# Kernel optimization log

Measured on AMD Instinct MI355X. Metric: run time of the kernel, lower is better.

## Reference

```python
import jax, jax.numpy as jnp
import numpy as np

B, T, N, C = 1, 2, 10000, 64
H, Co = 4, 64
E = 160000
NEG_SLOPE = 0.2
LN_EPS = 1e-5


def setup_inputs() -> dict:
    key = jax.random.key(0)
    ks = jax.random.split(key, 8)
    s_in = 1.0 / np.sqrt(C)
    s_att = 1.0 / np.sqrt(Co)
    s_proj = 1.0 / np.sqrt(H * Co)
    return {
        "x": jax.random.normal(ks[0], (B, T, N, C), jnp.float32),
        "edge_index": jax.random.randint(ks[1], (2, E), 0, N, dtype=jnp.int32),
        "W_l": jax.random.normal(ks[2], (C, H * Co), jnp.float32) * s_in,
        "b_l": jnp.zeros((H * Co,), jnp.float32),
        "W_r": jax.random.normal(ks[3], (C, H * Co), jnp.float32) * s_in,
        "b_r": jnp.zeros((H * Co,), jnp.float32),
        "att": jax.random.normal(ks[4], (H, Co), jnp.float32) * s_att,
        "bias": jnp.zeros((H * Co,), jnp.float32),
        "W_proj": jax.random.normal(ks[5], (H * Co, Co), jnp.float32) * s_proj,
        "b_proj": jnp.zeros((Co,), jnp.float32),
        "ln_gamma": jnp.ones((Co,), jnp.float32),
        "ln_beta": jnp.zeros((Co,), jnp.float32),
    }


def reference(x, edge_index, W_l, b_l, W_r, b_r, att, bias, W_proj, b_proj, ln_gamma, ln_beta):
    src, dst = edge_index[0], edge_index[1]
    # node transforms: [B,T,N,H,Co]
    x_l = (x @ W_l + b_l).reshape(B, T, N, H, Co)
    x_r = (x @ W_r + b_r).reshape(B, T, N, H, Co)
    # per-edge gathers: [B,T,E,H,Co]
    x_j = x_l[:, :, src]  # source-side features (messages)
    x_i = x_r[:, :, dst]  # target-side features
    m = jax.nn.leaky_relu(x_i + x_j, NEG_SLOPE)
    alpha = jnp.einsum('bteho,ho->bteh', m, att)  # [B,T,E,H]
    # segment softmax over edges grouped by target node (edge axis leading)
    a = jnp.moveaxis(alpha, 2, 0)  # [E,B,T,H]
    amax = jax.lax.stop_gradient(jax.ops.segment_max(a, dst, num_segments=N))
    a = jnp.exp(a - amax[dst])
    denom = jax.ops.segment_sum(a, dst, num_segments=N)
    attn = a / denom[dst]  # [E,B,T,H]
    # weighted messages scattered to target nodes
    msg = jnp.moveaxis(x_j, 2, 0) * attn[..., None]  # [E,B,T,H,Co]
    agg = jax.ops.segment_sum(msg, dst, num_segments=N)  # [N,B,T,H,Co]
    out = jnp.moveaxis(agg, 0, 2).reshape(B, T, N, H * Co) + bias
    x_mha = jax.nn.relu(out)
    # projection + identity residual (in_channels == out_channels)
    x_sam = x_mha @ W_proj + b_proj + x
    mu = jnp.mean(x_sam, axis=-1, keepdims=True)
    var = jnp.var(x_sam, axis=-1, keepdims=True)
    y = (x_sam - mu) * jax.lax.rsqrt(var + LN_EPS) * ln_gamma + ln_beta
    return jax.nn.relu(y)
```

## Files before the change

### kernel.cpp

```cpp
#include <hip/hip_runtime.h>

#define T_  2
#define N_  10000
#define C_  64
#define H_  4
#define Co_ 64
#define E_  160000
#define HC_ 256
#define PAD_ 48
#define NEG_SLOPE 0.2f
#define LN_EPS 1e-5f
#define SCAT_BLOCKS (E_ / 256)
#define GEMM_BLOCKS (T_ * N_ / 32)

__device__ __forceinline__ float lrelu(float v) {
    return fmaxf(v, NEG_SLOPE * v);
}
__device__ __forceinline__ float bf2f(unsigned short u) {
    return __uint_as_float((unsigned)u << 16);
}
__device__ __forceinline__ unsigned short f2bf(float f) {
    const unsigned u = __float_as_uint(f);
    return (unsigned short)((u + 0x7FFFu + ((u >> 16) & 1u)) >> 16);
}
__device__ __forceinline__ float4 u2f4(ushort4 u) {
    return make_float4(bf2f(u.x), bf2f(u.y), bf2f(u.z), bf2f(u.w));
}
__device__ __forceinline__ float red16(float x) {
    x += __int_as_float(__builtin_amdgcn_mov_dpp(__float_as_int(x), 0xB1,  0xF, 0xF, true));
    x += __int_as_float(__builtin_amdgcn_mov_dpp(__float_as_int(x), 0x4E,  0xF, 0xF, true));
    x += __int_as_float(__builtin_amdgcn_mov_dpp(__float_as_int(x), 0x141, 0xF, 0xF, true));
    x += __int_as_float(__builtin_amdgcn_mov_dpp(__float_as_int(x), 0x140, 0xF, 0xF, true));
    return x;
}
__device__ __forceinline__ float edot(const float4 xi, const float4 av, const float4 c) {
    float p =      lrelu(xi.x + c.x) * av.x;
    p = fmaf(lrelu(xi.y + c.y), av.y, p);
    p = fmaf(lrelu(xi.z + c.z), av.z, p);
    p = fmaf(lrelu(xi.w + c.w), av.w, p);
    return p;
}
__device__ __forceinline__ void group_update(
        const float4 xi, const float4 av,
        const float4 c0, const float4 c1, const float4 c2, const float4 c3,
        int k, int cnt, float& m, float& s, float4& acc) {
    float p0 = red16(edot(xi, av, c0));
    float p1 = red16(edot(xi, av, c1));
    float p2 = red16(edot(xi, av, c2));
    float p3 = red16(edot(xi, av, c3));
    if (k + 1 >= cnt) p1 = -INFINITY;
    if (k + 2 >= cnt) p2 = -INFINITY;
    if (k + 3 >= cnt) p3 = -INFINITY;
    const float gm = fmaxf(fmaxf(p0, p1), fmaxf(p2, p3));
    const float mn = fmaxf(m, gm);
    const float sc = __expf(m - mn);
    const float w0 = __expf(p0 - mn);
    const float w1 = __expf(p1 - mn);
    const float w2 = __expf(p2 - mn);
    const float w3 = __expf(p3 - mn);
    s = fmaf(s, sc, w0 + w1 + w2 + w3);
    acc.x = fmaf(acc.x, sc, fmaf(w0, c0.x, fmaf(w1, c1.x, fmaf(w2, c2.x, w3 * c3.x))));
    acc.y = fmaf(acc.y, sc, fmaf(w0, c0.y, fmaf(w1, c1.y, fmaf(w2, c2.y, w3 * c3.y))));
    acc.z = fmaf(acc.z, sc, fmaf(w0, c0.z, fmaf(w1, c1.z, fmaf(w2, c2.z, w3 * c3.z))));
    acc.w = fmaf(acc.w, sc, fmaf(w0, c0.w, fmaf(w1, c1.w, fmaf(w2, c2.w, w3 * c3.w))));
    m = mn;
}

__global__ __launch_bounds__(256) void scat_gemm(
        const int* __restrict__ src, const int* __restrict__ dst,
        int* __restrict__ cursor, unsigned short* __restrict__ perm,
        const float* __restrict__ x, const float* __restrict__ Wl,
        const float* __restrict__ bl, const float* __restrict__ Wr,
        const float* __restrict__ br, unsigned short* __restrict__ xlb,
        float* __restrict__ xr) {
    __shared__ float4 xs[32 * 16];
    const int tid = threadIdx.x;
    if (blockIdx.x < SCAT_BLOCKS) {
        const int e = blockIdx.x * 256 + tid;
        const int d = dst[e];
        const int pos = atomicAdd(&cursor[d], 1);
        if (pos < PAD_) perm[d * PAD_ + pos] = (unsigned short)src[e];
        return;
    }
    const int r0 = (blockIdx.x - SCAT_BLOCKS) * 32;
    xs[tid]       = ((const float4*)(x + (size_t)r0 * C_))[tid];
    xs[256 + tid] = ((const float4*)(x + (size_t)r0 * C_))[256 + tid];
    __syncthreads();

    const int wv    = tid >> 6;
    const int mat   = wv >> 1;
    const int rbase = (wv & 1) << 4;
    const int col4  = tid & 63;
    const float* W  = mat ? Wr : Wl;
    const float4 b4 = ((const float4*)(mat ? br : bl))[col4];

    float4 acc[16];
    #pragma unroll
    for (int r = 0; r < 16; ++r) acc[r] = b4;

    #pragma unroll 2
    for (int c4 = 0; c4 < 16; ++c4) {
        const float4 w0 = ((const float4*)(W + (size_t)(c4 * 4 + 0) * HC_))[col4];
        const float4 w1 = ((const float4*)(W + (size_t)(c4 * 4 + 1) * HC_))[col4];
        const float4 w2 = ((const float4*)(W + (size_t)(c4 * 4 + 2) * HC_))[col4];
        const float4 w3 = ((const float4*)(W + (size_t)(c4 * 4 + 3) * HC_))[col4];
        #pragma unroll
        for (int r = 0; r < 16; ++r) {
            const float4 xv = xs[(rbase + r) * 16 + c4];
            acc[r].x = fmaf(xv.x, w0.x, acc[r].x);
            acc[r].y = fmaf(xv.x, w0.y, acc[r].y);
            acc[r].z = fmaf(xv.x, w0.z, acc[r].z);
            acc[r].w = fmaf(xv.x, w0.w, acc[r].w);
            acc[r].x = fmaf(xv.y, w1.x, acc[r].x);
            acc[r].y = fmaf(xv.y, w1.y, acc[r].y);
            acc[r].z = fmaf(xv.y, w1.z, acc[r].z);
            acc[r].w = fmaf(xv.y, w1.w, acc[r].w);
            acc[r].x = fmaf(xv.z, w2.x, acc[r].x);
            acc[r].y = fmaf(xv.z, w2.y, acc[r].y);
            acc[r].z = fmaf(xv.z, w2.z, acc[r].z);
            acc[r].w = fmaf(xv.z, w2.w, acc[r].w);
            acc[r].x = fmaf(xv.w, w3.x, acc[r].x);
            acc[r].y = fmaf(xv.w, w3.y, acc[r].y);
            acc[r].z = fmaf(xv.w, w3.z, acc[r].z);
            acc[r].w = fmaf(xv.w, w3.w, acc[r].w);
        }
    }
    if (mat) {
        #pragma unroll
        for (int r = 0; r < 16; ++r)
            ((float4*)(xr + (size_t)(r0 + rbase + r) * HC_))[col4] = acc[r];
    } else {
        #pragma unroll
        for (int r = 0; r < 16; ++r) {
            ushort4 u;
            u.x = f2bf(acc[r].x); u.y = f2bf(acc[r].y);
            u.z = f2bf(acc[r].z); u.w = f2bf(acc[r].w);
            ((ushort4*)(xlb + (size_t)(r0 + rbase + r) * HC_))[col4] = u;
        }
    }
}

__global__ __launch_bounds__(256) void node_agg(
        const unsigned short* __restrict__ xlb, const float* __restrict__ xr,
        const float* __restrict__ att, const unsigned short* __restrict__ perm,
        const int* __restrict__ cursor, unsigned short* __restrict__ aggb) {
    const int n    = blockIdx.x * 4 + (threadIdx.x >> 6);
    const int lane = threadIdx.x & 63;
    const int deg  = min(cursor[n], PAD_);
    const float4 av  = ((const float4*)att)[lane];
    const float4 xi0 = ((const float4*)&xr[(size_t)n * HC_])[lane];
    const float4 xi1 = ((const float4*)&xr[((size_t)N_ + n) * HC_])[lane];
    const int myidx  = (lane < deg) ? (int)perm[n * PAD_ + lane] : 0;
    const unsigned short* xl1 = xlb + (size_t)N_ * HC_;

    float m0 = -INFINITY, s0 = 0.f;
    float m1 = -INFINITY, s1 = 0.f;
    float4 a0 = make_float4(0.f, 0.f, 0.f, 0.f);
    float4 a1 = make_float4(0.f, 0.f, 0.f, 0.f);

    ushort4 b00, b01, b02, b03, b10, b11, b12, b13;
    {
        const int i0 = __builtin_amdgcn_readlane(myidx, 0);
        const int i1 = __builtin_amdgcn_readlane(myidx, 1);
        const int i2 = __builtin_amdgcn_readlane(myidx, 2);
        const int i3 = __builtin_amdgcn_readlane(myidx, 3);
        b00 = ((const ushort4*)&xlb[(size_t)i0 * HC_])[lane];
        b01 = ((const ushort4*)&xlb[(size_t)i1 * HC_])[lane];
        b02 = ((const ushort4*)&xlb[(size_t)i2 * HC_])[lane];
        b03 = ((const ushort4*)&xlb[(size_t)i3 * HC_])[lane];
        b10 = ((const ushort4*)&xl1[(size_t)i0 * HC_])[lane];
        b11 = ((const ushort4*)&xl1[(size_t)i1 * HC_])[lane];
        b12 = ((const ushort4*)&xl1[(size_t)i2 * HC_])[lane];
        b13 = ((const ushort4*)&xl1[(size_t)i3 * HC_])[lane];
    }
    for (int k = 0; k < deg; k += 4) {
        const float4 c00 = u2f4(b00), c01 = u2f4(b01), c02 = u2f4(b02), c03 = u2f4(b03);
        const float4 c10 = u2f4(b10), c11 = u2f4(b11), c12 = u2f4(b12), c13 = u2f4(b13);
        if (k + 4 < deg) {
            const int i0 = __builtin_amdgcn_readlane(myidx, k + 4);
            const int i1 = __builtin_amdgcn_readlane(myidx, k + 5);
            const int i2 = __builtin_amdgcn_readlane(myidx, k + 6);
            const int i3 = __builtin_amdgcn_readlane(myidx, k + 7);
            b00 = ((const ushort4*)&xlb[(size_t)i0 * HC_])[lane];
            b01 = ((const ushort4*)&xlb[(size_t)i1 * HC_])[lane];
            b02 = ((const ushort4*)&xlb[(size_t)i2 * HC_])[lane];
            b03 = ((const ushort4*)&xlb[(size_t)i3 * HC_])[lane];
            b10 = ((const ushort4*)&xl1[(size_t)i0 * HC_])[lane];
            b11 = ((const ushort4*)&xl1[(size_t)i1 * HC_])[lane];
            b12 = ((const ushort4*)&xl1[(size_t)i2 * HC_])[lane];
            b13 = ((const ushort4*)&xl1[(size_t)i3 * HC_])[lane];
        }
        group_update(xi0, av, c00, c01, c02, c03, k, deg, m0, s0, a0);
        group_update(xi1, av, c10, c11, c12, c13, k, deg, m1, s1, a1);
    }
    if (deg > 0) {
        float inv = 1.f / s0;
        a0.x *= inv; a0.y *= inv; a0.z *= inv; a0.w *= inv;
        inv = 1.f / s1;
        a1.x *= inv; a1.y *= inv; a1.z *= inv; a1.w *= inv;
    }
    ushort4 o;
    o.x = f2bf(a0.x); o.y = f2bf(a0.y); o.z = f2bf(a0.z); o.w = f2bf(a0.w);
    ((ushort4*)&aggb[(size_t)n * HC_])[lane] = o;
    o.x = f2bf(a1.x); o.y = f2bf(a1.y); o.z = f2bf(a1.z); o.w = f2bf(a1.w);
    ((ushort4*)&aggb[((size_t)N_ + n) * HC_])[lane] = o;
}

__global__ __launch_bounds__(256) void epilogue(
        const unsigned short* __restrict__ aggb, const float* __restrict__ bias,
        const float* __restrict__ Wp, const float* __restrict__ bp,
        const float* __restrict__ x, const float* __restrict__ gamma,
        const float* __restrict__ beta, float* __restrict__ out) {
    __shared__ float sh[32 * HC_];
    const int r0  = blockIdx.x * 32;
    const int tid = threadIdx.x;
    #pragma unroll
    for (int i = 0; i < 8; ++i) {
        const int slot = i * 256 + tid;
        const int r = slot >> 6, f4 = slot & 63;
        const ushort4 u = ((const ushort4*)&aggb[(size_t)(r0 + r) * HC_])[f4];
        const float4 b = ((const float4*)bias)[f4];
        float4 v;
        v.x = fmaxf(bf2f(u.x) + b.x, 0.f); v.y = fmaxf(bf2f(u.y) + b.y, 0.f);
        v.z = fmaxf(bf2f(u.z) + b.z, 0.f); v.w = fmaxf(bf2f(u.w) + b.w, 0.f);
        ((float4*)sh)[slot] = v;
    }
    __syncthreads();
    const int wave = tid >> 6, o = tid & 63;
    const int rbase = wave * 8;
    const float bpo = bp[o];
    float acc[8];
    #pragma unroll
    for (int r = 0; r < 8; ++r)
        acc[r] = bpo + x[(size_t)(r0 + rbase + r) * C_ + o];
    for (int k = 0; k < HC_; k += 4) {
        const float w0 = Wp[(k + 0) * Co_ + o];
        const float w1 = Wp[(k + 1) * Co_ + o];
        const float w2 = Wp[(k + 2) * Co_ + o];
        const float w3 = Wp[(k + 3) * Co_ + o];
        #pragma unroll
        for (int r = 0; r < 8; ++r) {
            const float4 s4 = ((const float4*)&sh[(rbase + r) * HC_])[k >> 2];
            acc[r] = fmaf(s4.x, w0, acc[r]);
            acc[r] = fmaf(s4.y, w1, acc[r]);
            acc[r] = fmaf(s4.z, w2, acc[r]);
            acc[r] = fmaf(s4.w, w3, acc[r]);
        }
    }
    const float go = gamma[o], bo = beta[o];
    #pragma unroll
    for (int r = 0; r < 8; ++r) {
        float s1 = acc[r];
        #pragma unroll
        for (int off = 1; off < 64; off <<= 1) s1 += __shfl_xor(s1, off, 64);
        const float mu = s1 * (1.f / 64.f);
        const float dv = acc[r] - mu;
        float s2 = dv * dv;
        #pragma unroll
        for (int off = 1; off < 64; off <<= 1) s2 += __shfl_xor(s2, off, 64);
        const float var = s2 * (1.f / 64.f);
        const float y = dv * rsqrtf(var + LN_EPS) * go + bo;
        out[(size_t)(r0 + rbase + r) * C_ + o] = fmaxf(y, 0.f);
    }
}

extern "C" void kernel_launch(void* const* d_in, const int* in_sizes, int n_in,
                              void* d_out, int out_size, void* d_ws, size_t ws_size,
                              hipStream_t stream) {
    const float* x    = (const float*)d_in[0];
    const int*   ei   = (const int*)  d_in[1];
    const float* Wl   = (const float*)d_in[2];
    const float* bl   = (const float*)d_in[3];
    const float* Wr   = (const float*)d_in[4];
    const float* br   = (const float*)d_in[5];
    const float* att  = (const float*)d_in[6];
    const float* bias = (const float*)d_in[7];
    const float* Wp   = (const float*)d_in[8];
    const float* bp   = (const float*)d_in[9];
    const float* gam  = (const float*)d_in[10];
    const float* bet  = (const float*)d_in[11];
    const int* src = ei;
    const int* dst = ei + E_;

    char* ws = (char*)d_ws;
    unsigned short* xlb  = (unsigned short*)ws;
    float*          xr   = (float*)(xlb + (size_t)T_ * N_ * HC_);
    unsigned short* aggb = (unsigned short*)(xr + (size_t)T_ * N_ * HC_);
    int*            cursor = (int*)(aggb + (size_t)T_ * N_ * HC_);
    unsigned short* perm   = (unsigned short*)(cursor + N_);

    hipMemsetAsync(cursor, 0, N_ * sizeof(int), stream);
    scat_gemm<<<SCAT_BLOCKS + GEMM_BLOCKS, 256, 0, stream>>>(
        src, dst, cursor, perm, x, Wl, bl, Wr, br, xlb, xr);
    node_agg<<<N_ / 4, 256, 0, stream>>>(xlb, xr, att, perm, cursor, aggb);
    epilogue<<<T_ * N_ / 32, 256, 0, stream>>>(aggb, bias, Wp, bp, x,
                                               gam, bet, (float*)d_out);
}
```

Before: 172.2 us.

## Fuse node aggregation with projection and LayerNorm epilogue into one kernel

Merges node_agg and epilogue into a single node_proj kernel. Each wave now processes two nodes with a combined prefetch pipeline over both nodes' edge groups, then writes the biased, ReLU'd aggregates to shared memory and performs the projection, residual and LayerNorm directly. This removes the bf16 aggb round trip through global memory and one kernel launch. In exchange each wave reads all of Wp for only four rows instead of eight, so weight traffic per output rises. Register pressure also increases, constrained by launch_bounds(256,4).

```diff
diff --git a/kernel.cpp b/kernel.cpp
--- a/kernel.cpp
+++ b/kernel.cpp
@@ -140,127 +140,159 @@
     }
 }
 
-__global__ __launch_bounds__(256) void node_agg(
+__global__ __launch_bounds__(256, 4) void node_proj(
         const unsigned short* __restrict__ xlb, const float* __restrict__ xr,
         const float* __restrict__ att, const unsigned short* __restrict__ perm,
-        const int* __restrict__ cursor, unsigned short* __restrict__ aggb) {
-    const int n    = blockIdx.x * 4 + (threadIdx.x >> 6);
-    const int lane = threadIdx.x & 63;
-    const int deg  = min(cursor[n], PAD_);
-    const float4 av  = ((const float4*)att)[lane];
-    const float4 xi0 = ((const float4*)&xr[(size_t)n * HC_])[lane];
-    const float4 xi1 = ((const float4*)&xr[((size_t)N_ + n) * HC_])[lane];
-    const int myidx  = (lane < deg) ? (int)perm[n * PAD_ + lane] : 0;
-    const unsigned short* xl1 = xlb + (size_t)N_ * HC_;
-
-    float m0 = -INFINITY, s0 = 0.f;
-    float m1 = -INFINITY, s1 = 0.f;
-    float4 a0 = make_float4(0.f, 0.f, 0.f, 0.f);
-    float4 a1 = make_float4(0.f, 0.f, 0.f, 0.f);
-
-    ushort4 b00, b01, b02, b03, b10, b11, b12, b13;
-    {
-        const int i0 = __builtin_amdgcn_readlane(myidx, 0);
-        const int i1 = __builtin_amdgcn_readlane(myidx, 1);
-        const int i2 = __builtin_amdgcn_readlane(myidx, 2);
-        const int i3 = __builtin_amdgcn_readlane(myidx, 3);
-        b00 = ((const ushort4*)&xlb[(size_t)i0 * HC_])[lane];
-        b01 = ((const ushort4*)&xlb[(size_t)i1 * HC_])[lane];
-        b02 = ((const ushort4*)&xlb[(size_t)i2 * HC_])[lane];
-        b03 = ((const ushort4*)&xlb[(size_t)i3 * HC_])[lane];
-        b10 = ((const ushort4*)&xl1[(size_t)i0 * HC_])[lane];
-        b11 = ((const ushort4*)&xl1[(size_t)i1 * HC_])[lane];
-        b12 = ((const ushort4*)&xl1[(size_t)i2 * HC_])[lane];
-        b13 = ((const ushort4*)&xl1[(size_t)i3 * HC_])[lane];
-    }
-    for (int k = 0; k < deg; k += 4) {
-        const float4 c00 = u2f4(b00), c01 = u2f4(b01), c02 = u2f4(b02), c03 = u2f4(b03);
-        const float4 c10 = u2f4(b10), c11 = u2f4(b11), c12 = u2f4(b12), c13 = u2f4(b13);
-        if (k + 4 < deg) {
-            const int i0 = __builtin_amdgcn_readlane(myidx, k + 4);
-            const int i1 = __builtin_amdgcn_readlane(myidx, k + 5);
-            const int i2 = __builtin_amdgcn_readlane(myidx, k + 6);
-            const int i3 = __builtin_amdgcn_readlane(myidx, k + 7);
-            b00 = ((const ushort4*)&xlb[(size_t)i0 * HC_])[lane];
-            b01 = ((const ushort4*)&xlb[(size_t)i1 * HC_])[lane];
-            b02 = ((const ushort4*)&xlb[(size_t)i2 * HC_])[lane];
-            b03 = ((const ushort4*)&xlb[(size_t)i3 * HC_])[lane];
-            b10 = ((const ushort4*)&xl1[(size_t)i0 * HC_])[lane];
-            b11 = ((const ushort4*)&xl1[(size_t)i1 * HC_])[lane];
-            b12 = ((const ushort4*)&xl1[(size_t)i2 * HC_])[lane];
-            b13 = ((const ushort4*)&xl1[(size_t)i3 * HC_])[lane];
-        }
-        group_update(xi0, av, c00, c01, c02, c03, k, deg, m0, s0, a0);
-        group_update(xi1, av, c10, c11, c12, c13, k, deg, m1, s1, a1);
-    }
-    if (deg > 0) {
-        float inv = 1.f / s0;
-        a0.x *= inv; a0.y *= inv; a0.z *= inv; a0.w *= inv;
-        inv = 1.f / s1;
-        a1.x *= inv; a1.y *= inv; a1.z *= inv; a1.w *= inv;
-    }
-    ushort4 o;
-    o.x = f2bf(a0.x); o.y = f2bf(a0.y); o.z = f2bf(a0.z); o.w = f2bf(a0.w);
-    ((ushort4*)&aggb[(size_t)n * HC_])[lane] = o;
-    o.x = f2bf(a1.x); o.y = f2bf(a1.y); o.z = f2bf(a1.z); o.w = f2bf(a1.w);
-    ((ushort4*)&aggb[((size_t)N_ + n) * HC_])[lane] = o;
-}
-
-__global__ __launch_bounds__(256) void epilogue(
-        const unsigned short* __restrict__ aggb, const float* __restrict__ bias,
+        const int* __restrict__ cursor, const float* __restrict__ bias,
         const float* __restrict__ Wp, const float* __restrict__ bp,
         const float* __restrict__ x, const float* __restrict__ gamma,
         const float* __restrict__ beta, float* __restrict__ out) {
-    __shared__ float sh[32 * HC_];
-    const int r0  = blockIdx.x * 32;
-    const int tid = threadIdx.x;
-    #pragma unroll
-    for (int i = 0; i < 8; ++i) {
-        const int slot = i * 256 + tid;
-        const int r = slot >> 6, f4 = slot & 63;
-        const ushort4 u = ((const ushort4*)&aggb[(size_t)(r0 + r) * HC_])[f4];
-        const float4 b = ((const float4*)bias)[f4];
+    __shared__ float sh[4][4][HC_];
+    const int wv   = threadIdx.x >> 6;
+    const int lane = threadIdx.x & 63;
+    const int wid  = blockIdx.x * 4 + wv;
+    const int n0   = wid * 2, n1 = n0 + 1;
+    const int deg0 = min(cursor[n0], PAD_);
+    const int deg1 = min(cursor[n1], PAD_);
+    const float4 av   = ((const float4*)att)[lane];
+    const float4 xi00 = ((const float4*)&xr[(size_t)n0 * HC_])[lane];
+    const float4 xi01 = ((const float4*)&xr[((size_t)N_ + n0) * HC_])[lane];
+    const float4 xi10 = ((const float4*)&xr[(size_t)n1 * HC_])[lane];
+    const float4 xi11 = ((const float4*)&xr[((size_t)N_ + n1) * HC_])[lane];
+    const int idx0 = (lane < deg0) ? (int)perm[n0 * PAD_ + lane] : 0;
+    const int idx1 = (lane < deg1) ? (int)perm[n1 * PAD_ + lane] : 0;
+    const unsigned short* xl1 = xlb + (size_t)N_ * HC_;
+    const int g0 = (deg0 + 3) >> 2, g1 = (deg1 + 3) >> 2, gtot = g0 + g1;
+
+    float m00 = -INFINITY, s00 = 0.f, m01 = -INFINITY, s01 = 0.f;
+    float m10 = -INFINITY, s10 = 0.f, m11 = -INFINITY, s11 = 0.f;
+    float4 a00 = make_float4(0.f, 0.f, 0.f, 0.f), a01 = a00, a10 = a00, a11 = a00;
+
+    ushort4 b0, b1, b2, b3, b4, b5, b6, b7;
+    auto fetch = [&](int g) {
+        int idx, kk;
+        if (g < g0) { idx = idx0; kk = 4 * g; }
+        else        { idx = idx1; kk = 4 * (g - g0); }
+        const int i0 = __builtin_amdgcn_readlane(idx, kk + 0);
+        const int i1 = __builtin_amdgcn_readlane(idx, kk + 1);
+        const int i2 = __builtin_amdgcn_readlane(idx, kk + 2);
+        const int i3 = __builtin_amdgcn_readlane(idx, kk + 3);
+        b0 = ((const ushort4*)&xlb[(size_t)i0 * HC_])[lane];
+        b1 = ((const ushort4*)&xlb[(size_t)i1 * HC_])[lane];
+        b2 = ((const ushort4*)&xlb[(size_t)i2 * HC_])[lane];
+        b3 = ((const ushort4*)&xlb[(size_t)i3 * HC_])[lane];
+        b4 = ((const ushort4*)&xl1[(size_t)i0 * HC_])[lane];
+        b5 = ((const ushort4*)&xl1[(size_t)i1 * HC_])[lane];
+        b6 = ((const ushort4*)&xl1[(size_t)i2 * HC_])[lane];
+        b7 = ((const ushort4*)&xl1[(size_t)i3 * HC_])[lane];
+    };
+    if (gtot > 0) fetch(0);
+    for (int g = 0; g < gtot; ++g) {
+        const float4 c0 = u2f4(b0), c1 = u2f4(b1), c2 = u2f4(b2), c3 = u2f4(b3);
+        const float4 d0 = u2f4(b4), d1 = u2f4(b5), d2 = u2f4(b6), d3 = u2f4(b7);
+        if (g + 1 < gtot) fetch(g + 1);
+        if (g < g0) {
+            const int k = 4 * g;
+            group_update(xi00, av, c0, c1, c2, c3, k, deg0, m00, s00, a00);
+            group_update(xi01, av, d0, d1, d2, d3, k, deg0, m01, s01, a01);
+        } else {
+            const int k = 4 * (g - g0);
+            group_update(xi10, av, c0, c1, c2, c3, k, deg1, m10, s10, a10);
+            group_update(xi11, av, d0, d1, d2, d3, k, deg1, m11, s11, a11);
+        }
+    }
+
+    const float4 bias4 = ((const float4*)bias)[lane];
+    {
+        const float i0v = (deg0 > 0) ? 1.f / s00 : 0.f;
+        const float i1v = (deg0 > 0) ? 1.f / s01 : 0.f;
+        const float i2v = (deg1 > 0) ? 1.f / s10 : 0.f;
+        const float i3v = (deg1 > 0) ? 1.f / s11 : 0.f;
         float4 v;
-        v.x = fmaxf(bf2f(u.x) + b.x, 0.f); v.y = fmaxf(bf2f(u.y) + b.y, 0.f);
-        v.z = fmaxf(bf2f(u.z) + b.z, 0.f); v.w = fmaxf(bf2f(u.w) + b.w, 0.f);
-        ((float4*)sh)[slot] = v;
+        v.x = fmaxf(fmaf(a00.x, i0v, bias4.x), 0.f);
+        v.y = fmaxf(fmaf(a00.y, i0v, bias4.y), 0.f);
+        v.z = fmaxf(fmaf(a00.z, i0v, bias4.z), 0.f);
+        v.w = fmaxf(fmaf(a00.w, i0v, bias4.w), 0.f);
+        ((float4*)&sh[wv][0][0])[lane] = v;
+        v.x = fmaxf(fmaf(a01.x, i1v, bias4.x), 0.f);
+        v.y = fmaxf(fmaf(a01.y, i1v, bias4.y), 0.f);
+        v.z = fmaxf(fmaf(a01.z, i1v, bias4.z), 0.f);
+        v.w = fmaxf(fmaf(a01.w, i1v, bias4.w), 0.f);
+        ((float4*)&sh[wv][1][0])[lane] = v;
+        v.x = fmaxf(fmaf(a10.x, i2v, bias4.x), 0.f);
+        v.y = fmaxf(fmaf(a10.y, i2v, bias4.y), 0.f);
+        v.z = fmaxf(fmaf(a10.z, i2v, bias4.z), 0.f);
+        v.w = fmaxf(fmaf(a10.w, i2v, bias4.w), 0.f);
+        ((float4*)&sh[wv][2][0])[lane] = v;
+        v.x = fmaxf(fmaf(a11.x, i3v, bias4.x), 0.f);
+        v.y = fmaxf(fmaf(a11.y, i3v, bias4.y), 0.f);
+        v.z = fmaxf(fmaf(a11.z, i3v, bias4.z), 0.f);
+        v.w = fmaxf(fmaf(a11.w, i3v, bias4.w), 0.f);
+        ((float4*)&sh[wv][3][0])[lane] = v;
     }
     __syncthreads();
-    const int wave = tid >> 6, o = tid & 63;
-    const int rbase = wave * 8;
+
+    const int o = lane;
     const float bpo = bp[o];
-    float acc[8];
-    #pragma unroll
-    for (int r = 0; r < 8; ++r)
-        acc[r] = bpo + x[(size_t)(r0 + rbase + r) * C_ + o];
-    for (int k = 0; k < HC_; k += 4) {
-        const float w0 = Wp[(k + 0) * Co_ + o];
-        const float w1 = Wp[(k + 1) * Co_ + o];
-        const float w2 = Wp[(k + 2) * Co_ + o];
-        const float w3 = Wp[(k + 3) * Co_ + o];
-        #pragma unroll
-        for (int r = 0; r < 8; ++r) {
-            const float4 s4 = ((const float4*)&sh[(rbase + r) * HC_])[k >> 2];
-            acc[r] = fmaf(s4.x, w0, acc[r]);
-            acc[r] = fmaf(s4.y, w1, acc[r]);
-            acc[r] = fmaf(s4.z, w2, acc[r]);
-            acc[r] = fmaf(s4.w, w3, acc[r]);
-        }
-    }
+    float p0 = bpo + x[(size_t)n0 * C_ + o];
+    float p1 = bpo + x[((size_t)N_ + n0) * C_ + o];
+    float p2 = bpo + x[(size_t)n1 * C_ + o];
+    float p3 = bpo + x[((size_t)N_ + n1) * C_ + o];
+    #pragma unroll 4
+    for (int k4 = 0; k4 < 64; ++k4) {
+        const float w0 = Wp[(k4 * 4 + 0) * Co_ + o];
+        const float w1 = Wp[(k4 * 4 + 1) * Co_ + o];
+        const float w2 = Wp[(k4 * 4 + 2) * Co_ + o];
+        const float w3 = Wp[(k4 * 4 + 3) * Co_ + o];
+        const float4 s0 = ((const float4*)&sh[wv][0][0])[k4];
+        const float4 s1 = ((const float4*)&sh[wv][1][0])[k4];
+        const float4 s2 = ((const float4*)&sh[wv][2][0])[k4];
+        const float4 s3 = ((const float4*)&sh[wv][3][0])[k4];
+        p0 = fmaf(s0.x, w0, p0); p0 = fmaf(s0.y, w1, p0);
+        p0 = fmaf(s0.z, w2, p0); p0 = fmaf(s0.w, w3, p0);
+        p1 = fmaf(s1.x, w0, p1); p1 = fmaf(s1.y, w1, p1);
+        p1 = fmaf(s1.z, w2, p1); p1 = fmaf(s1.w, w3, p1);
+        p2 = fmaf(s2.x, w0, p2); p2 = fmaf(s2.y, w1, p2);
+        p2 = fmaf(s2.z, w2, p2); p2 = fmaf(s2.w, w3, p2);
+        p3 = fmaf(s3.x, w0, p3); p3 = fmaf(s3.y, w1, p3);
+        p3 = fmaf(s3.z, w2, p3); p3 = fmaf(s3.w, w3, p3);
+    }
+
     const float go = gamma[o], bo = beta[o];
-    #pragma unroll
-    for (int r = 0; r < 8; ++r) {
-        float s1 = acc[r];
-        #pragma unroll
-        for (int off = 1; off < 64; off <<= 1) s1 += __shfl_xor(s1, off, 64);
-        const float mu = s1 * (1.f / 64.f);
-        const float dv = acc[r] - mu;
-        float s2 = dv * dv;
-        #pragma unroll
-        for (int off = 1; off < 64; off <<= 1) s2 += __shfl_xor(s2, off, 64);
-        const float var = s2 * (1.f / 64.f);
-        const float y = dv * rsqrtf(var + LN_EPS) * go + bo;
-        out[(size_t)(r0 + rbase + r) * C_ + o] = fmaxf(y, 0.f);
+    {
+        float v, s1r, s2r, mu, dv;
+        v = p0; s1r = v;
+        #pragma unroll
+        for (int off = 1; off < 64; off <<= 1) s1r += __shfl_xor(s1r, off, 64);
+        mu = s1r * (1.f / 64.f); dv = v - mu; s2r = dv * dv;
+        #pragma unroll
+        for (int off = 1; off < 64; off <<= 1) s2r += __shfl_xor(s2r, off, 64);
+        out[(size_t)n0 * C_ + o] =
+            fmaxf(dv * rsqrtf(s2r * (1.f / 64.f) + LN_EPS) * go + bo, 0.f);
+        v = p1; s1r = v;
+        #pragma unroll
+        for (int off = 1; off < 64; off <<= 1) s1r += __shfl_xor(s1r, off, 64);
+        mu = s1r * (1.f / 64.f); dv = v - mu; s2r = dv * dv;
+        #pragma unroll
+        for (int off = 1; off < 64; off <<= 1) s2r += __shfl_xor(s2r, off, 64);
+        out[((size_t)N_ + n0) * C_ + o] =
+            fmaxf(dv * rsqrtf(s2r * (1.f / 64.f) + LN_EPS) * go + bo, 0.f);
+        v = p2; s1r = v;
+        #pragma unroll
+        for (int off = 1; off < 64; off <<= 1) s1r += __shfl_xor(s1r, off, 64);
+        mu = s1r * (1.f / 64.f); dv = v - mu; s2r = dv * dv;
+        #pragma unroll
+        for (int off = 1; off < 64; off <<= 1) s2r += __shfl_xor(s2r, off, 64);
+        out[(size_t)n1 * C_ + o] =
+            fmaxf(dv * rsqrtf(s2r * (1.f / 64.f) + LN_EPS) * go + bo, 0.f);
+        v = p3; s1r = v;
+        #pragma unroll
+        for (int off = 1; off < 64; off <<= 1) s1r += __shfl_xor(s1r, off, 64);
+        mu = s1r * (1.f / 64.f); dv = v - mu; s2r = dv * dv;
+        #pragma unroll
+        for (int off = 1; off < 64; off <<= 1) s2r += __shfl_xor(s2r, off, 64);
+        out[((size_t)N_ + n1) * C_ + o] =
+            fmaxf(dv * rsqrtf(s2r * (1.f / 64.f) + LN_EPS) * go + bo, 0.f);
     }
 }
 
@@ -285,14 +317,12 @@
     char* ws = (char*)d_ws;
     unsigned short* xlb  = (unsigned short*)ws;
     float*          xr   = (float*)(xlb + (size_t)T_ * N_ * HC_);
-    unsigned short* aggb = (unsigned short*)(xr + (size_t)T_ * N_ * HC_);
-    int*            cursor = (int*)(aggb + (size_t)T_ * N_ * HC_);
+    int*            cursor = (int*)(xr + (size_t)T_ * N_ * HC_);
     unsigned short* perm   = (unsigned short*)(cursor + N_);
 
     hipMemsetAsync(cursor, 0, N_ * sizeof(int), stream);
     scat_gemm<<<SCAT_BLOCKS + GEMM_BLOCKS, 256, 0, stream>>>(
         src, dst, cursor, perm, x, Wl, bl, Wr, br, xlb, xr);
-    node_agg<<<N_ / 4, 256, 0, stream>>>(xlb, xr, att, perm, cursor, aggb);
-    epilogue<<<T_ * N_ / 32, 256, 0, stream>>>(aggb, bias, Wp, bp, x,
-                                               gam, bet, (float*)d_out);
-}
+    node_proj<<<N_ / 8, 256, 0, stream>>>(xlb, xr, att, perm, cursor, bias,
+                                          Wp, bp, x, gam, bet, (float*)d_out);
+}
```

Measured after the change: 167.4 us. 1.03x faster.

## Fuse node aggregation with projection and LayerNorm, use packed FMA math

Applied to the files above, without the earlier changes.

Merges the node aggregation and epilogue kernels into one. Each wave now projects its own node's aggregated features through W_proj and applies LayerNorm directly, so the bf16 aggregate buffer is no longer written to and re-read from global memory, and one launch is removed. The edge attention dot products and accumulator updates are rewritten with packed two-wide float FMAs, and a single inline-asm DPP sequence interleaves four reductions. The trade-off is that the projection now reuses each W_proj load across only two rows per wave instead of eight, which adds global/L2 weight traffic. The fused kernel also carries extra register pressure under a tighter launch bound.

```diff
diff --git a/kernel.cpp b/kernel.cpp
--- a/kernel.cpp
+++ b/kernel.cpp
@@ -13,9 +13,17 @@
 #define SCAT_BLOCKS (E_ / 256)
 #define GEMM_BLOCKS (T_ * N_ / 32)
 
-__device__ __forceinline__ float lrelu(float v) {
-    return fmaxf(v, NEG_SLOPE * v);
-}
+typedef float v2f __attribute__((ext_vector_type(2)));
+
+#if __has_builtin(__builtin_elementwise_fma)
+#define PKFMA(a, b, c) __builtin_elementwise_fma((a), (b), (c))
+#else
+#define PKFMA(a, b, c) ((a) * (b) + (c))
+#endif
+
+__device__ __forceinline__ v2f v2(float x, float y) { v2f r; r.x = x; r.y = y; return r; }
+__device__ __forceinline__ v2f sp(float x) { v2f r; r.x = x; r.y = x; return r; }
+
 __device__ __forceinline__ float bf2f(unsigned short u) {
     return __uint_as_float((unsigned)u << 16);
 }
@@ -26,28 +34,47 @@
 __device__ __forceinline__ float4 u2f4(ushort4 u) {
     return make_float4(bf2f(u.x), bf2f(u.y), bf2f(u.z), bf2f(u.w));
 }
-__device__ __forceinline__ float red16(float x) {
-    x += __int_as_float(__builtin_amdgcn_mov_dpp(__float_as_int(x), 0xB1,  0xF, 0xF, true));
-    x += __int_as_float(__builtin_amdgcn_mov_dpp(__float_as_int(x), 0x4E,  0xF, 0xF, true));
-    x += __int_as_float(__builtin_amdgcn_mov_dpp(__float_as_int(x), 0x141, 0xF, 0xF, true));
-    x += __int_as_float(__builtin_amdgcn_mov_dpp(__float_as_int(x), 0x140, 0xF, 0xF, true));
-    return x;
-}
-__device__ __forceinline__ float edot(const float4 xi, const float4 av, const float4 c) {
-    float p =      lrelu(xi.x + c.x) * av.x;
-    p = fmaf(lrelu(xi.y + c.y), av.y, p);
-    p = fmaf(lrelu(xi.z + c.z), av.z, p);
-    p = fmaf(lrelu(xi.w + c.w), av.w, p);
-    return p;
-}
+
+__device__ __forceinline__ void red16x4(float& p0, float& p1, float& p2, float& p3) {
+    asm("s_nop 1\n\t"
+        "v_add_f32_dpp %0, %0, %0 quad_perm:[1,0,3,2] row_mask:0xf bank_mask:0xf\n\t"
+        "v_add_f32_dpp %1, %1, %1 quad_perm:[1,0,3,2] row_mask:0xf bank_mask:0xf\n\t"
+        "v_add_f32_dpp %2, %2, %2 quad_perm:[1,0,3,2] row_mask:0xf bank_mask:0xf\n\t"
+        "v_add_f32_dpp %3, %3, %3 quad_perm:[1,0,3,2] row_mask:0xf bank_mask:0xf\n\t"
+        "v_add_f32_dpp %0, %0, %0 quad_perm:[2,3,0,1] row_mask:0xf bank_mask:0xf\n\t"
+        "v_add_f32_dpp %1, %1, %1 quad_perm:[2,3,0,1] row_mask:0xf bank_mask:0xf\n\t"
+        "v_add_f32_dpp %2, %2, %2 quad_perm:[2,3,0,1] row_mask:0xf bank_mask:0xf\n\t"
+        "v_add_f32_dpp %3, %3, %3 quad_perm:[2,3,0,1] row_mask:0xf bank_mask:0xf\n\t"
+        "v_add_f32_dpp %0, %0, %0 row_half_mirror row_mask:0xf bank_mask:0xf\n\t"
+        "v_add_f32_dpp %1, %1, %1 row_half_mirror row_mask:0xf bank_mask:0xf\n\t"
+        "v_add_f32_dpp %2, %2, %2 row_half_mirror row_mask:0xf bank_mask:0xf\n\t"
+        "v_add_f32_dpp %3, %3, %3 row_half_mirror row_mask:0xf bank_mask:0xf\n\t"
+        "v_add_f32_dpp %0, %0, %0 row_mirror row_mask:0xf bank_mask:0xf\n\t"
+        "v_add_f32_dpp %1, %1, %1 row_mirror row_mask:0xf bank_mask:0xf\n\t"
+        "v_add_f32_dpp %2, %2, %2 row_mirror row_mask:0xf bank_mask:0xf\n\t"
+        "v_add_f32_dpp %3, %3, %3 row_mirror row_mask:0xf bank_mask:0xf"
+        : "+v"(p0), "+v"(p1), "+v"(p2), "+v"(p3));
+}
+
+__device__ __forceinline__ float edot2(const v2f xa, const v2f xb,
+                                       const v2f aa, const v2f ab, const float4 c) {
+    v2f u = v2(c.x, c.y) + xa;
+    v2f v = v2(c.z, c.w) + xb;
+    v2f lu = __builtin_elementwise_max(u, u * 0.2f);
+    v2f lv = __builtin_elementwise_max(v, v * 0.2f);
+    v2f p = PKFMA(lv, ab, lu * aa);
+    return p.x + p.y;
+}
+
 __device__ __forceinline__ void group_update(
-        const float4 xi, const float4 av,
+        const v2f xa, const v2f xb, const v2f aa, const v2f ab,
         const float4 c0, const float4 c1, const float4 c2, const float4 c3,
         int k, int cnt, float& m, float& s, float4& acc) {
-    float p0 = red16(edot(xi, av, c0));
-    float p1 = red16(edot(xi, av, c1));
-    float p2 = red16(edot(xi, av, c2));
-    float p3 = red16(edot(xi, av, c3));
+    float p0 = edot2(xa, xb, aa, ab, c0);
+    float p1 = edot2(xa, xb, aa, ab, c1);
+    float p2 = edot2(xa, xb, aa, ab, c2);
+    float p3 = edot2(xa, xb, aa, ab, c3);
+    red16x4(p0, p1, p2, p3);
     if (k + 1 >= cnt) p1 = -INFINITY;
     if (k + 2 >= cnt) p2 = -INFINITY;
     if (k + 3 >= cnt) p3 = -INFINITY;
@@ -59,10 +86,17 @@
     const float w2 = __expf(p2 - mn);
     const float w3 = __expf(p3 - mn);
     s = fmaf(s, sc, w0 + w1 + w2 + w3);
-    acc.x = fmaf(acc.x, sc, fmaf(w0, c0.x, fmaf(w1, c1.x, fmaf(w2, c2.x, w3 * c3.x))));
-    acc.y = fmaf(acc.y, sc, fmaf(w0, c0.y, fmaf(w1, c1.y, fmaf(w2, c2.y, w3 * c3.y))));
-    acc.z = fmaf(acc.z, sc, fmaf(w0, c0.z, fmaf(w1, c1.z, fmaf(w2, c2.z, w3 * c3.z))));
-    acc.w = fmaf(acc.w, sc, fmaf(w0, c0.w, fmaf(w1, c1.w, fmaf(w2, c2.w, w3 * c3.w))));
+    v2f q01 = v2(c3.x, c3.y) * w3;
+    q01 = PKFMA(v2(c2.x, c2.y), sp(w2), q01);
+    q01 = PKFMA(v2(c1.x, c1.y), sp(w1), q01);
+    q01 = PKFMA(v2(c0.x, c0.y), sp(w0), q01);
+    v2f r01 = PKFMA(v2(acc.x, acc.y), sp(sc), q01);
+    v2f q23 = v2(c3.z, c3.w) * w3;
+    q23 = PKFMA(v2(c2.z, c2.w), sp(w2), q23);
+    q23 = PKFMA(v2(c1.z, c1.w), sp(w1), q23);
+    q23 = PKFMA(v2(c0.z, c0.w), sp(w0), q23);
+    v2f r23 = PKFMA(v2(acc.z, acc.w), sp(sc), q23);
+    acc.x = r01.x; acc.y = r01.y; acc.z = r23.x; acc.w = r23.y;
     m = mn;
 }
 
@@ -140,12 +174,17 @@
     }
 }
 
-__global__ __launch_bounds__(256) void node_agg(
+__global__ __launch_bounds__(256, 8) void node_proj(
         const unsigned short* __restrict__ xlb, const float* __restrict__ xr,
         const float* __restrict__ att, const unsigned short* __restrict__ perm,
-        const int* __restrict__ cursor, unsigned short* __restrict__ aggb) {
-    const int n    = blockIdx.x * 4 + (threadIdx.x >> 6);
+        const int* __restrict__ cursor, const float* __restrict__ bias,
+        const float* __restrict__ Wp, const float* __restrict__ bp,
+        const float* __restrict__ x, const float* __restrict__ gamma,
+        const float* __restrict__ beta, float* __restrict__ out) {
+    __shared__ float sh[4][2][HC_];
+    const int wv   = threadIdx.x >> 6;
     const int lane = threadIdx.x & 63;
+    const int n    = blockIdx.x * 4 + wv;
     const int deg  = min(cursor[n], PAD_);
     const float4 av  = ((const float4*)att)[lane];
     const float4 xi0 = ((const float4*)&xr[(size_t)n * HC_])[lane];
@@ -153,114 +192,99 @@
     const int myidx  = (lane < deg) ? (int)perm[n * PAD_ + lane] : 0;
     const unsigned short* xl1 = xlb + (size_t)N_ * HC_;
 
-    float m0 = -INFINITY, s0 = 0.f;
-    float m1 = -INFINITY, s1 = 0.f;
-    float4 a0 = make_float4(0.f, 0.f, 0.f, 0.f);
-    float4 a1 = make_float4(0.f, 0.f, 0.f, 0.f);
-
-    ushort4 b00, b01, b02, b03, b10, b11, b12, b13;
+    const v2f xa = v2(xi0.x, xi0.y), xb = v2(xi0.z, xi0.w);
+    const v2f ya = v2(xi1.x, xi1.y), yb = v2(xi1.z, xi1.w);
+    const v2f aa = v2(av.x, av.y),   ab = v2(av.z, av.w);
+
+    float m0 = -INFINITY, s0 = 0.f, m1 = -INFINITY, s1 = 0.f;
+    float4 a0 = make_float4(0.f, 0.f, 0.f, 0.f), a1 = a0;
+
+    ushort4 b0, b1, b2, b3, b4, b5, b6, b7;
+    auto fetch = [&](int kk) {
+        const int i0 = __builtin_amdgcn_readlane(myidx, kk + 0);
+        const int i1 = __builtin_amdgcn_readlane(myidx, kk + 1);
+        const int i2 = __builtin_amdgcn_readlane(myidx, kk + 2);
+        const int i3 = __builtin_amdgcn_readlane(myidx, kk + 3);
+        b0 = ((const ushort4*)&xlb[(size_t)i0 * HC_])[lane];
+        b1 = ((const ushort4*)&xlb[(size_t)i1 * HC_])[lane];
+        b2 = ((const ushort4*)&xlb[(size_t)i2 * HC_])[lane];
+        b3 = ((const ushort4*)&xlb[(size_t)i3 * HC_])[lane];
+        b4 = ((const ushort4*)&xl1[(size_t)i0 * HC_])[lane];
+        b5 = ((const ushort4*)&xl1[(size_t)i1 * HC_])[lane];
+        b6 = ((const ushort4*)&xl1[(size_t)i2 * HC_])[lane];
+        b7 = ((const ushort4*)&xl1[(size_t)i3 * HC_])[lane];
+    };
+    if (deg > 0) fetch(0);
+    for (int k = 0; k < deg; k += 4) {
+        const float4 c0 = u2f4(b0), c1 = u2f4(b1), c2 = u2f4(b2), c3 = u2f4(b3);
+        const float4 d0 = u2f4(b4), d1 = u2f4(b5), d2 = u2f4(b6), d3 = u2f4(b7);
+        if (k + 4 < deg) fetch(k + 4);
+        group_update(xa, xb, aa, ab, c0, c1, c2, c3, k, deg, m0, s0, a0);
+        group_update(ya, yb, aa, ab, d0, d1, d2, d3, k, deg, m1, s1, a1);
+    }
+
+    const float4 bias4 = ((const float4*)bias)[lane];
     {
-        const int i0 = __builtin_amdgcn_readlane(myidx, 0);
-        const int i1 = __builtin_amdgcn_readlane(myidx, 1);
-        const int i2 = __builtin_amdgcn_readlane(myidx, 2);
-        const int i3 = __builtin_amdgcn_readlane(myidx, 3);
-        b00 = ((const ushort4*)&xlb[(size_t)i0 * HC_])[lane];
-        b01 = ((const ushort4*)&xlb[(size_t)i1 * HC_])[lane];
-        b02 = ((const ushort4*)&xlb[(size_t)i2 * HC_])[lane];
-        b03 = ((const ushort4*)&xlb[(size_t)i3 * HC_])[lane];
-        b10 = ((const ushort4*)&xl1[(size_t)i0 * HC_])[lane];
-        b11 = ((const ushort4*)&xl1[(size_t)i1 * HC_])[lane];
-        b12 = ((const ushort4*)&xl1[(size_t)i2 * HC_])[lane];
-        b13 = ((const ushort4*)&xl1[(size_t)i3 * HC_])[lane];
-    }
-    for (int k = 0; k < deg; k += 4) {
-        const float4 c00 = u2f4(b00), c01 = u2f4(b01), c02 = u2f4(b02), c03 = u2f4(b03);
-        const float4 c10 = u2f4(b10), c11 = u2f4(b11), c12 = u2f4(b12), c13 = u2f4(b13);
-        if (k + 4 < deg) {
-            const int i0 = __builtin_amdgcn_readlane(myidx, k + 4);
-            const int i1 = __builtin_amdgcn_readlane(myidx, k + 5);
-            const int i2 = __builtin_amdgcn_readlane(myidx, k + 6);
-            const int i3 = __builtin_amdgcn_readlane(myidx, k + 7);
-            b00 = ((const ushort4*)&xlb[(size_t)i0 * HC_])[lane];
-            b01 = ((const ushort4*)&xlb[(size_t)i1 * HC_])[lane];
-            b02 = ((const ushort4*)&xlb[(size_t)i2 * HC_])[lane];
-            b03 = ((const ushort4*)&xlb[(size_t)i3 * HC_])[lane];
-            b10 = ((const ushort4*)&xl1[(size_t)i0 * HC_])[lane];
-            b11 = ((const ushort4*)&xl1[(size_t)i1 * HC_])[lane];
-            b12 = ((const ushort4*)&xl1[(size_t)i2 * HC_])[lane];
-            b13 = ((const ushort4*)&xl1[(size_t)i3 * HC_])[lane];
-        }
-        group_update(xi0, av, c00, c01, c02, c03, k, deg, m0, s0, a0);
-        group_update(xi1, av, c10, c11, c12, c13, k, deg, m1, s1, a1);
-    }
-    if (deg > 0) {
-        float inv = 1.f / s0;
-        a0.x *= inv; a0.y *= inv; a0.z *= inv; a0.w *= inv;
-        inv = 1.f / s1;
-        a1.x *= inv; a1.y *= inv; a1.z *= inv; a1.w *= inv;
-    }
-    ushort4 o;
-    o.x = f2bf(a0.x); o.y = f2bf(a0.y); o.z = f2bf(a0.z); o.w = f2bf(a0.w);
-    ((ushort4*)&aggb[(size_t)n * HC_])[lane] = o;
-    o.x = f2bf(a1.x); o.y = f2bf(a1.y); o.z = f2bf(a1.z); o.w = f2bf(a1.w);
-    ((ushort4*)&aggb[((size_t)N_ + n) * HC_])[lane] = o;
-}
-
-__global__ __launch_bounds__(256) void epilogue(
-        const unsigned short* __restrict__ aggb, const float* __restrict__ bias,
-        const float* __restrict__ Wp, const float* __restrict__ bp,
-        const float* __restrict__ x, const float* __restrict__ gamma,
-        const float* __restrict__ beta, float* __restrict__ out) {
-    __shared__ float sh[32 * HC_];
-    const int r0  = blockIdx.x * 32;
-    const int tid = threadIdx.x;
-    #pragma unroll
-    for (int i = 0; i < 8; ++i) {
-        const int slot = i * 256 + tid;
-        const int r = slot >> 6, f4 = slot & 63;
-        const ushort4 u = ((const ushort4*)&aggb[(size_t)(r0 + r) * HC_])[f4];
-        const float4 b = ((const float4*)bias)[f4];
+        const float i0v = (deg > 0) ? 1.f / s0 : 0.f;
+        const float i1v = (deg > 0) ? 1.f / s1 : 0.f;
         float4 v;
-        v.x = fmaxf(bf2f(u.x) + b.x, 0.f); v.y = fmaxf(bf2f(u.y) + b.y, 0.f);
-        v.z = fmaxf(bf2f(u.z) + b.z, 0.f); v.w = fmaxf(bf2f(u.w) + b.w, 0.f);
-        ((float4*)sh)[slot] = v;
-    }
-    __syncthreads();
-    const int wave = tid >> 6, o = tid & 63;
-    const int rbase = wave * 8;
-    const float bpo = bp[o];
-    float acc[8];
-    #pragma unroll
-    for (int r = 0; r < 8; ++r)
-        acc[r] = bpo + x[(size_t)(r0 + rbase + r) * C_ + o];
+        v.x = fmaxf(fmaf(a0.x, i0v, bias4.x), 0.f);
+        v.y = fmaxf(fmaf(a0.y, i0v, bias4.y), 0.f);
+        v.z = fmaxf(fmaf(a0.z, i0v, bias4.z), 0.f);
+        v.w = fmaxf(fmaf(a0.w, i0v, bias4.w), 0.f);
+        ((float4*)&sh[wv][0][0])[lane] = v;
+        v.x = fmaxf(fmaf(a1.x, i1v, bias4.x), 0.f);
+        v.y = fmaxf(fmaf(a1.y, i1v, bias4.y), 0.f);
+        v.z = fmaxf(fmaf(a1.z, i1v, bias4.z), 0.f);
+        v.w = fmaxf(fmaf(a1.w, i1v, bias4.w), 0.f);
+        ((float4*)&sh[wv][1][0])[lane] = v;
+    }
+    asm volatile("s_waitcnt lgkmcnt(0)" ::: "memory");
+
+    const int o = lane;
+    const float* sh0 = &sh[wv][0][0];
+    const float* sh1 = &sh[wv][1][0];
+    v2f P0 = v2(0.f, 0.f), P1 = v2(0.f, 0.f);
+    #pragma unroll 4
     for (int k = 0; k < HC_; k += 4) {
         const float w0 = Wp[(k + 0) * Co_ + o];
         const float w1 = Wp[(k + 1) * Co_ + o];
         const float w2 = Wp[(k + 2) * Co_ + o];
         const float w3 = Wp[(k + 3) * Co_ + o];
-        #pragma unroll
-        for (int r = 0; r < 8; ++r) {
-            const float4 s4 = ((const float4*)&sh[(rbase + r) * HC_])[k >> 2];
-            acc[r] = fmaf(s4.x, w0, acc[r]);
-            acc[r] = fmaf(s4.y, w1, acc[r]);
-            acc[r] = fmaf(s4.z, w2, acc[r]);
-            acc[r] = fmaf(s4.w, w3, acc[r]);
-        }
-    }
+        const float4 s0v = ((const float4*)sh0)[k >> 2];
+        const float4 s1v = ((const float4*)sh1)[k >> 2];
+        P0 = PKFMA(v2(s0v.x, s0v.y), v2(w0, w1), P0);
+        P0 = PKFMA(v2(s0v.z, s0v.w), v2(w2, w3), P0);
+        P1 = PKFMA(v2(s1v.x, s1v.y), v2(w0, w1), P1);
+        P1 = PKFMA(v2(s1v.z, s1v.w), v2(w2, w3), P1);
+    }
+    const float bpo = bp[o];
+    float p0 = P0.x + P0.y + bpo + x[(size_t)n * C_ + o];
+    float p1 = P1.x + P1.y + bpo + x[((size_t)N_ + n) * C_ + o];
+
     const float go = gamma[o], bo = beta[o];
-    #pragma unroll
-    for (int r = 0; r < 8; ++r) {
-        float s1 = acc[r];
-        #pragma unroll
-        for (int off = 1; off < 64; off <<= 1) s1 += __shfl_xor(s1, off, 64);
-        const float mu = s1 * (1.f / 64.f);
-        const float dv = acc[r] - mu;
-        float s2 = dv * dv;
-        #pragma unroll
-        for (int off = 1; off < 64; off <<= 1) s2 += __shfl_xor(s2, off, 64);
-        const float var = s2 * (1.f / 64.f);
-        const float y = dv * rsqrtf(var + LN_EPS) * go + bo;
-        out[(size_t)(r0 + rbase + r) * C_ + o] = fmaxf(y, 0.f);
+    {
+        float s1r = p0;
+        #pragma unroll
+        for (int off = 1; off < 64; off <<= 1) s1r += __shfl_xor(s1r, off, 64);
+        const float mu0 = s1r * (1.f / 64.f);
+        const float dv0 = p0 - mu0;
+        float s2r = dv0 * dv0;
+        #pragma unroll
+        for (int off = 1; off < 64; off <<= 1) s2r += __shfl_xor(s2r, off, 64);
+        out[(size_t)n * C_ + o] =
+            fmaxf(dv0 * rsqrtf(s2r * (1.f / 64.f) + LN_EPS) * go + bo, 0.f);
+
+        float t1r = p1;
+        #pragma unroll
+        for (int off = 1; off < 64; off <<= 1) t1r += __shfl_xor(t1r, off, 64);
+        const float mu1 = t1r * (1.f / 64.f);
+        const float dv1 = p1 - mu1;
+        float t2r = dv1 * dv1;
+        #pragma unroll
+        for (int off = 1; off < 64; off <<= 1) t2r += __shfl_xor(t2r, off, 64);
+        out[((size_t)N_ + n) * C_ + o] =
+            fmaxf(dv1 * rsqrtf(t2r * (1.f / 64.f) + LN_EPS) * go + bo, 0.f);
     }
 }
 
@@ -285,14 +309,12 @@
     char* ws = (char*)d_ws;
     unsigned short* xlb  = (unsigned short*)ws;
     float*          xr   = (float*)(xlb + (size_t)T_ * N_ * HC_);
-    unsigned short* aggb = (unsigned short*)(xr + (size_t)T_ * N_ * HC_);
-    int*            cursor = (int*)(aggb + (size_t)T_ * N_ * HC_);
+    int*            cursor = (int*)(xr + (size_t)T_ * N_ * HC_);
     unsigned short* perm   = (unsigned short*)(cursor + N_);
 
     hipMemsetAsync(cursor, 0, N_ * sizeof(int), stream);
     scat_gemm<<<SCAT_BLOCKS + GEMM_BLOCKS, 256, 0, stream>>>(
         src, dst, cursor, perm, x, Wl, bl, Wr, br, xlb, xr);
-    node_agg<<<N_ / 4, 256, 0, stream>>>(xlb, xr, att, perm, cursor, aggb);
-    epilogue<<<T_ * N_ / 32, 256, 0, stream>>>(aggb, bias, Wp, bp, x,
-                                               gam, bet, (float*)d_out);
-}
+    node_proj<<<N_ / 4, 256, 0, stream>>>(xlb, xr, att, perm, cursor, bias,
+                                          Wp, bp, x, gam, bet, (float*)d_out);
+}
```

New measurement: 232.4 us. 1.35x slower.
